# Kernel optimization log

Measured on AMD Instinct MI355X. Metric: run time of the kernel, lower is better.

Reference implementation:

```python
import jax, jax.numpy as jnp
import numpy as np

B, N, L, D = 1, 128, 256, 256   # batch, num_seqs, seq_len, msa_dim
P, H = 128, 8                   # pair_dim, num_heads
DH = D // H                     # head_dim


def setup_inputs() -> dict:
    key = jax.random.key(0)
    ks = jax.random.split(key, 7)
    msa = jax.random.normal(ks[0], (B, N, L, D), dtype=jnp.float32)
    pair = jax.random.normal(ks[1], (B, L, L, P), dtype=jnp.float32)
    mask = jax.random.randint(ks[2], (B, N, L), 0, 2) > 0  # bool key mask
    w_qkv = jax.random.normal(ks[3], (D, 3 * D), dtype=jnp.float32) * (D ** -0.5)
    w_pb = jax.random.normal(ks[4], (P, H), dtype=jnp.float32) * (P ** -0.5)
    b_pb = jnp.zeros((H,), dtype=jnp.float32)
    w_out = jax.random.normal(ks[5], (D, D), dtype=jnp.float32) * (D ** -0.5)
    b_out = jnp.zeros((D,), dtype=jnp.float32)
    return {"msa": msa, "pair": pair, "mask": mask, "w_qkv": w_qkv,
            "w_pb": w_pb, "b_pb": b_pb, "w_out": w_out, "b_out": b_out}


def reference(msa, pair, mask, w_qkv, w_pb, b_pb, w_out, b_out):
    b, n, l, d = msa.shape
    scaling = DH ** -0.5
    qkv = msa @ w_qkv                                   # [b,n,l,3d]
    qkv = qkv.reshape(b, n, l, 3, H, DH)
    q, k, v = qkv[..., 0, :, :], qkv[..., 1, :, :], qkv[..., 2, :, :]  # [b,n,l,h,dh]
    pair_bias = (pair @ w_pb + b_pb)                    # [b,l,l,h]
    pair_bias = jnp.transpose(pair_bias, (0, 3, 1, 2))  # [b,h,l,l]
    # scores: [b,n,h,l,l]
    dots = jnp.einsum('bnqhd,bnkhd->bnhqk', q, k) * scaling
    dots = dots + pair_bias[:, None]                    # broadcast over num_seqs
    dots = jnp.where(mask[:, :, None, None, :], dots, -jnp.inf)  # mask keys
    attn = jax.nn.softmax(dots, axis=-1)
    out = jnp.einsum('bnhqk,bnkhd->bnqhd', attn, v)     # [b,n,l,h,dh]
    out = out.reshape(b, n, l, d)
    return out @ w_out + b_out
```

## Files before the change

kernel.cpp:

```cpp
#include <hip/hip_runtime.h>
#include <hip/hip_bf16.h>

#define NN 128
#define LL 256
#define DD 256
#define PP 128
#define HH 8
#define DHH 32

typedef __bf16 bf16x8 __attribute__((ext_vector_type(8)));
typedef short s16x4 __attribute__((ext_vector_type(4)));
typedef float f32x4 __attribute__((ext_vector_type(4)));
typedef unsigned int u32x2 __attribute__((ext_vector_type(2)));

__device__ __forceinline__ void gload_lds16(const void* g, void* l) {
  __builtin_amdgcn_global_load_lds(
      (const __attribute__((address_space(1))) void*)g,
      (__attribute__((address_space(3))) void*)l, 16, 0, 0);
}

__global__ __launch_bounds__(256) void cvt_bf16(
    const float* __restrict__ src, __hip_bfloat16* __restrict__ dst, int n) {
  for (int i = (blockIdx.x * 256 + threadIdx.x) * 4; i < n; i += gridDim.x * 1024) {
    float4 v = *(const float4*)(src + i);
    ushort4 o;
    o.x = __bfloat16_as_ushort(__float2bfloat16(v.x));
    o.y = __bfloat16_as_ushort(__float2bfloat16(v.y));
    o.z = __bfloat16_as_ushort(__float2bfloat16(v.z));
    o.w = __bfloat16_as_ushort(__float2bfloat16(v.w));
    *(ushort4*)(dst + i) = o;
  }
}

__global__ __launch_bounds__(256) void transpose_cvt(
    const float* __restrict__ src, __hip_bfloat16* __restrict__ dst,
    int K, int N) {
  __shared__ float t[32][33];
  int n0 = blockIdx.x * 32, k0 = blockIdx.y * 32;
  int tx = threadIdx.x & 31, ty = threadIdx.x >> 5;
  for (int i = 0; i < 4; ++i) {
    int ky = ty + i * 8;
    t[ky][tx] = src[(size_t)(k0 + ky) * N + n0 + tx];
  }
  __syncthreads();
  for (int i = 0; i < 4; ++i) {
    int ny = ty + i * 8;
    dst[(size_t)(n0 + ny) * K + k0 + tx] = __float2bfloat16(t[tx][ny]);
  }
}

#define MODE_I32 0
#define MODE_I8 1
#define MODE_BF16 2
#define MODE_F32 3

__global__ __launch_bounds__(256) void mask_expand(
    const unsigned char* __restrict__ mraw, float* __restrict__ mout) {
  __shared__ int s_or1, s_or2, s_or3, s_max, s_mode;
  int tid = threadIdx.x;
  if (tid == 0) { s_or1 = 0; s_or2 = 0; s_or3 = 0; s_max = 0; }
  __syncthreads();
  int or1 = 0, or2 = 0, or3 = 0, mx = 0;
  for (int j = tid; j < 4096; j += 256) {
    int b = mraw[j];
    mx = mx > b ? mx : b;
    int r = j & 3;
    if (r == 1) or1 |= b;
    else if (r == 2) or2 |= b;
    else if (r == 3) or3 |= b;
  }
  atomicOr(&s_or1, or1); atomicOr(&s_or2, or2); atomicOr(&s_or3, or3);
  atomicMax(&s_max, mx);
  __syncthreads();
  if (tid == 0) {
    int mode;
    if (s_max <= 1) mode = ((s_or1 | s_or2 | s_or3) == 0) ? MODE_I32 : MODE_I8;
    else            mode = (s_or1 != 0) ? MODE_BF16 : MODE_F32;
    s_mode = mode;
  }
  __syncthreads();
  int mode = s_mode;
  int i0 = blockIdx.x * 1024;
  for (int i = i0 + tid; i < i0 + 1024; i += 256) {
    int v;
    if (mode == MODE_I32)       v = ((const int*)mraw)[i] != 0;
    else if (mode == MODE_I8)   v = mraw[i] != 0;
    else if (mode == MODE_BF16) v = ((const unsigned short*)mraw)[i] != 0;
    else                        v = ((const unsigned int*)mraw)[i] != 0;
    mout[i] = v ? 1.f : 0.f;
  }
}

#define GEMM_MAINLOOP(Aptr, Btptr)                                            \
  __shared__ __align__(16) __hip_bfloat16 Asm[128 * 32];                      \
  __shared__ __align__(16) __hip_bfloat16 Bsm[128 * 32];                      \
  int tid = threadIdx.x;                                                      \
  int lane = tid & 63;                                                        \
  int wv = tid >> 6;                                                          \
  int wm = (wv >> 1) * 64, wn = (wv & 1) * 64;                                \
  int lr = lane & 15, quad = lane >> 4;                                       \
  int bm = blockIdx.x, bn = blockIdx.y;                                       \
  f32x4 acc[4][4];                                                            \
  for (int i = 0; i < 4; ++i)                                                 \
    for (int j = 0; j < 4; ++j) acc[i][j] = (f32x4){0.f, 0.f, 0.f, 0.f};      \
  for (int ks = 0; ks < 8; ++ks) {                                            \
    int k0 = ks * 32;                                                         \
    if (ks) __syncthreads();                                                  \
    for (int i = 0; i < 2; ++i) {                                             \
      int c = tid + i * 256;                                                  \
      int row = c >> 2, cc = c & 3;                                           \
      int ldsbase = (wv * 64 + i * 256) * 8;      \
      gload_lds16(Aptr + ((size_t)(bm * 128 + row)) * 256 + k0 + cc * 8,      \
                  Asm + ldsbase);                                             \
      gload_lds16(Btptr + ((size_t)(bn * 128 + row)) * 256 + k0 + cc * 8,     \
                  Bsm + ldsbase);                                             \
    }                                                                         \
    __syncthreads();                                                          \
    bf16x8 af[4], bfr[4];                                                     \
    for (int mi = 0; mi < 4; ++mi)                                            \
      af[mi] = *(const bf16x8*)&Asm[(wm + mi * 16 + lr) * 32 + quad * 8];     \
    for (int ni = 0; ni < 4; ++ni)                                            \
      bfr[ni] = *(const bf16x8*)&Bsm[(wn + ni * 16 + lr) * 32 + quad * 8];    \
    for (int mi = 0; mi < 4; ++mi)                                            \
      for (int ni = 0; ni < 4; ++ni)                                          \
        acc[mi][ni] = __builtin_amdgcn_mfma_f32_16x16x32_bf16(                \
            af[mi], bfr[ni], acc[mi][ni], 0, 0, 0);                           \
  }

__global__ __launch_bounds__(256) void qkv_gemm_mfma(
    const __hip_bfloat16* __restrict__ A,
    const __hip_bfloat16* __restrict__ Bt,
    __hip_bfloat16* __restrict__ qb,
    __hip_bfloat16* __restrict__ kb,
    __hip_bfloat16* __restrict__ vb) {
  GEMM_MAINLOOP(A, Bt)
  for (int mi = 0; mi < 4; ++mi) {
    for (int ni = 0; ni < 4; ++ni) {
      int gcol = bn * 128 + wn + ni * 16 + lr;
      int t = gcol >> 8, rem = gcol & 255;
      int h = rem >> 5, dh = rem & 31;
      for (int r = 0; r < 4; ++r) {
        int grow = bm * 128 + wm + mi * 16 + quad * 4 + r;
        int n = grow >> 8, l = grow & 255;
        __hip_bfloat16 val = __float2bfloat16(acc[mi][ni][r]);
        if (t == 0)
          qb[(size_t)(((n * HH + h) * LL + l)) * DHH + dh] = val;
        else if (t == 1)
          kb[(size_t)(((n * HH + h) * LL + l)) * DHH + dh] = val;
        else
          vb[(size_t)(((n * HH + h) * DHH + dh)) * LL + l] = val;
      }
    }
  }
}

__global__ __launch_bounds__(256) void out_gemm_mfma(
    const __hip_bfloat16* __restrict__ A,
    const __hip_bfloat16* __restrict__ Bt,
    const float* __restrict__ bout,
    float* __restrict__ C) {
  GEMM_MAINLOOP(A, Bt)
  for (int mi = 0; mi < 4; ++mi) {
    for (int ni = 0; ni < 4; ++ni) {
      int gcol = bn * 128 + wn + ni * 16 + lr;
      float bo = bout[gcol];
      for (int r = 0; r < 4; ++r) {
        int grow = bm * 128 + wm + mi * 16 + quad * 4 + r;
        C[(size_t)grow * 256 + gcol] = acc[mi][ni][r] + bo;
      }
    }
  }
}

__global__ __launch_bounds__(256) void pair_bias_kernel(
    const float* __restrict__ pair,
    const float* __restrict__ w_pb,
    const float* __restrict__ b_pb,
    __hip_bfloat16* __restrict__ expb) {
  __shared__ float wp[128][9];
  __shared__ float rows[32][129];
  int tid = threadIdx.x;
  for (int i = 0; i < 4; ++i) {
    int e = tid + i * 256;
    wp[e >> 3][e & 7] = w_pb[e];
  }
  int row0 = blockIdx.x * 32;
  const float* src = pair + (size_t)row0 * PP;
  for (int i = 0; i < 16; ++i) {
    int e = tid + i * 256;
    int r = e >> 7, c = e & 127;
    rows[r][c] = src[r * 128 + c];
  }
  __syncthreads();
  int h = tid >> 5, rl = tid & 31;
  float acc = b_pb[h] - 12.0f;
  for (int p = 0; p < 128; ++p)
    acc += rows[rl][p] * wp[p][h];
  int row = row0 + rl;
  int i = row >> 8, j = row & 255;
  expb[((size_t)(h * LL + i)) * LL + j] = __float2bfloat16(__expf(acc));
}

__global__ __launch_bounds__(256, 2) void attn_mfma(
    const __hip_bfloat16* __restrict__ qb,
    const __hip_bfloat16* __restrict__ kb,
    const __hip_bfloat16* __restrict__ vbt,
    const __hip_bfloat16* __restrict__ expb,
    const float* __restrict__ maskf,
    __hip_bfloat16* __restrict__ ao) {
  int bx = blockIdx.x;
  int h = bx >> 7, n = bx & 127;
  int nh = n * HH + h;
  int tid = threadIdx.x, lane = tid & 63, wv = tid >> 6;
  int lr = lane & 15, quad = lane >> 4;
  int wm = wv * 64;
  size_t base = (size_t)nh * (LL * DHH);

  const __hip_bfloat16* qp = qb + base;
  const __hip_bfloat16* kp = kb + base;
  const __hip_bfloat16* vp = vbt + base;
  const __hip_bfloat16* ep = expb + (size_t)h * LL * LL;
  const float* mrow = maskf + n * LL;

  const float cs = 0.17677669529663687f * 1.4426950408889634f;

  bf16x8 aq[4];
#pragma unroll
  for (int mi = 0; mi < 4; ++mi)
    aq[mi] = *(const bf16x8*)(qp + (size_t)(wm + mi * 16 + lr) * DHH + quad * 8);

  bf16x8 bkA[4], bkB[4];
  s16x4 avA[4][2], avB[4][2];
  f32x4 mwA[4], mwB[4];
  uint2 ebE[4], ebO[4];

#define LOADKT(S, KT)                                                          \
  {                                                                            \
    const int j0_ = (KT) * 64;                                                 \
    _Pragma("unroll") for (int nj = 0; nj < 4; ++nj)                           \
        bk##S[nj] =                                                            \
        *(const bf16x8*)(kp + (size_t)(j0_ + nj * 16 + lr) * DHH + quad * 8);  \
    _Pragma("unroll") for (int nj = 0; nj < 4; ++nj) {                         \
      av##S[nj][0] = *(const s16x4*)(vp + (size_t)lr * LL +                    \
                                     j0_ + nj * 16 + quad * 4);                \
      av##S[nj][1] = *(const s16x4*)(vp + (size_t)(16 + lr) * LL +             \
                                     j0_ + nj * 16 + quad * 4);                \
    }                                                                          \
    _Pragma("unroll") for (int nj = 0; nj < 4; ++nj)                           \
        mw##S[nj] = *(const f32x4*)(mrow + j0_ + nj * 16 + quad * 4);          \
  }

#define LOADEB(S, KT, MI)                                                      \
  {                                                                            \
    const __hip_bfloat16* er_ =                                                \
        ep + (size_t)(wm + (MI) * 16 + lr) * LL + (KT) * 64;                   \
    _Pragma("unroll") for (int nj = 0; nj < 4; ++nj)                           \
        eb##S[nj] = *(const uint2*)(er_ + nj * 16 + quad * 4);                 \
  }

#define MI_PHASE(KT, MI, C, EC, EN, NKT, NMI, DOPF)                            \
  {                                                                            \
    if (DOPF) LOADEB(EN, NKT, NMI);                                            \
    f32x4 s_[4];                                                               \
    _Pragma("unroll") for (int nj = 0; nj < 4; ++nj)                           \
        s_[nj] = __builtin_amdgcn_mfma_f32_16x16x32_bf16(                      \
            bk##C[nj], aq[MI], (f32x4){0.f, 0.f, 0.f, 0.f}, 0, 0, 0);          \
    _Pragma("unroll") for (int nj = 0; nj < 4; ++nj) {                         \
      uint2 e_ = eb##EC[nj];                                                   \
      f32x4 m4_ = mw##C[nj];                                                   \
      float em0_ = __uint_as_float(e_.x << 16) * m4_[0];                       \
      float em1_ = __uint_as_float(e_.x & 0xffff0000u) * m4_[1];               \
      float em2_ = __uint_as_float(e_.y << 16) * m4_[2];                       \
      float em3_ = __uint_as_float(e_.y & 0xffff0000u) * m4_[3];               \
      float p0_ = exp2f(s_[nj][0] * cs) * em0_;                                \
      float p1_ = exp2f(s_[nj][1] * cs) * em1_;                                \
      float p2_ = exp2f(s_[nj][2] * cs) * em2_;                                \
      float p3_ = exp2f(s_[nj][3] * cs) * em3_;                                \
      lsum[MI] += (p0_ + p1_) + (p2_ + p3_);                                   \
      unsigned lo_ =                                                           \
          ((unsigned)__bfloat16_as_ushort(__float2bfloat16(p1_)) << 16) |      \
          (unsigned)__bfloat16_as_ushort(__float2bfloat16(p0_));               \
      unsigned hi_ =                                                           \
          ((unsigned)__bfloat16_as_ushort(__float2bfloat16(p3_)) << 16) |      \
          (unsigned)__bfloat16_as_ushort(__float2bfloat16(p2_));               \
      u32x2 pu_ = {lo_, hi_};                                                  \
      s16x4 pb_ = __builtin_bit_cast(s16x4, pu_);                              \
      o_acc[MI][0] = __builtin_amdgcn_mfma_f32_16x16x16bf16_1k(                \
          av##C[nj][0], pb_, o_acc[MI][0], 0, 0, 0);                           \
      o_acc[MI][1] = __builtin_amdgcn_mfma_f32_16x16x16bf16_1k(                \
          av##C[nj][1], pb_, o_acc[MI][1], 0, 0, 0);                           \
    }                                                                          \
  }

#define KT_PHASE(KT, C, N, LAST)                                               \
  {                                                                            \
    if (!(LAST)) LOADKT(N, (KT) + 1);                                          \
    MI_PHASE(KT, 0, C, E, O, KT, 1, 1)                                         \
    MI_PHASE(KT, 1, C, O, E, KT, 2, 1)                                         \
    MI_PHASE(KT, 2, C, E, O, KT, 3, 1)                                         \
    MI_PHASE(KT, 3, C, O, E, (KT) + 1 > 3 ? 0 : (KT) + 1, 0, !(LAST))          \
  }

  float lsum[4] = {0.f, 0.f, 0.f, 0.f};
  f32x4 o_acc[4][2];
#pragma unroll
  for (int mi = 0; mi < 4; ++mi)
#pragma unroll
    for (int no = 0; no < 2; ++no) o_acc[mi][no] = (f32x4){0.f, 0.f, 0.f, 0.f};

  LOADKT(A, 0)
  LOADEB(E, 0, 0)

  KT_PHASE(0, A, B, 0)
  KT_PHASE(1, B, A, 0)
  KT_PHASE(2, A, B, 0)
  KT_PHASE(3, B, A, 1)

#undef LOADKT
#undef LOADEB
#undef MI_PHASE
#undef KT_PHASE

#pragma unroll
  for (int mi = 0; mi < 4; ++mi) {
    float ls = lsum[mi];
    ls += __shfl_xor(ls, 16);
    ls += __shfl_xor(ls, 32);
    float inv = (ls > 0.f) ? 1.f / ls : 0.f;
    int q = wm + mi * 16 + lr;
#pragma unroll
    for (int no = 0; no < 2; ++no) {
      f32x4 o = o_acc[mi][no];
      ushort4 w;
      w.x = __bfloat16_as_ushort(__float2bfloat16(o[0] * inv));
      w.y = __bfloat16_as_ushort(__float2bfloat16(o[1] * inv));
      w.z = __bfloat16_as_ushort(__float2bfloat16(o[2] * inv));
      w.w = __bfloat16_as_ushort(__float2bfloat16(o[3] * inv));
      *(ushort4*)(ao + (size_t)n * (LL * DD) + (size_t)q * DD +
                  h * DHH + no * 16 + quad * 4) = w;
    }
  }
}

extern "C" void kernel_launch(void* const* d_in, const int* in_sizes, int n_in,
                              void* d_out, int out_size, void* d_ws, size_t ws_size,
                              hipStream_t stream) {
  const float* msa   = (const float*)d_in[0];
  const float* pair  = (const float*)d_in[1];
  const unsigned char* mask = (const unsigned char*)d_in[2];
  const float* w_qkv = (const float*)d_in[3];
  const float* w_pb  = (const float*)d_in[4];
  const float* b_pb  = (const float*)d_in[5];
  const float* w_out = (const float*)d_in[6];
  const float* b_out = (const float*)d_in[7];
  float* out = (float*)d_out;

  char* ws = (char*)d_ws;
  __hip_bfloat16* qb      = (__hip_bfloat16*)(ws);
  __hip_bfloat16* kb      = (__hip_bfloat16*)(ws + 16777216);
  __hip_bfloat16* vb      = (__hip_bfloat16*)(ws + 33554432);
  __hip_bfloat16* msa_c   = (__hip_bfloat16*)(ws + 50331648);
  __hip_bfloat16* ao      = (__hip_bfloat16*)(ws + 50331648);
  __hip_bfloat16* expb    = (__hip_bfloat16*)(ws + 67108864);
  __hip_bfloat16* wqkv_t  = (__hip_bfloat16*)(ws + 71303168);
  __hip_bfloat16* wout_t  = (__hip_bfloat16*)(ws + 71696384);
  float*          msk     = (float*)(ws + 71827456);

  mask_expand<<<32, 256, 0, stream>>>(mask, msk);
  cvt_bf16<<<1024, 256, 0, stream>>>(msa, msa_c, NN * LL * DD);
  transpose_cvt<<<dim3(24, 8), 256, 0, stream>>>(w_qkv, wqkv_t, 256, 768);
  transpose_cvt<<<dim3(8, 8), 256, 0, stream>>>(w_out, wout_t, 256, 256);

  qkv_gemm_mfma<<<dim3(256, 6), 256, 0, stream>>>(msa_c, wqkv_t, qb, kb, vb);
  pair_bias_kernel<<<2048, 256, 0, stream>>>(pair, w_pb, b_pb, expb);
  attn_mfma<<<1024, 256, 0, stream>>>(qb, kb, vb, expb, msk, ao);
  out_gemm_mfma<<<dim3(256, 2), 256, 0, stream>>>(ao, wout_t, b_out, out);
}
```

Before: 252.9 us.

## Permute key index layout so attention loads use 16-byte vector reads

```diff
diff --git a/kernel.cpp b/kernel.cpp
--- a/kernel.cpp
+++ b/kernel.cpp
@@ -10,8 +10,13 @@
 
 typedef __bf16 bf16x8 __attribute__((ext_vector_type(8)));
 typedef short s16x4 __attribute__((ext_vector_type(4)));
+typedef short s16x8 __attribute__((ext_vector_type(8)));
 typedef float f32x4 __attribute__((ext_vector_type(4)));
 typedef unsigned int u32x2 __attribute__((ext_vector_type(2)));
+
+__device__ __forceinline__ int permk(int k) {
+  return (k & 0xC3) | ((k & 0x30) >> 2) | ((k & 0x0C) << 2);
+}
 
 __device__ __forceinline__ void gload_lds16(const void* g, void* l) {
   __builtin_amdgcn_global_load_lds(
@@ -87,7 +92,7 @@
     else if (mode == MODE_I8)   v = mraw[i] != 0;
     else if (mode == MODE_BF16) v = ((const unsigned short*)mraw)[i] != 0;
     else                        v = ((const unsigned int*)mraw)[i] != 0;
-    mout[i] = v ? 1.f : 0.f;
+    mout[(i & ~255) | permk(i & 255)] = v ? 1.f : 0.f;
   }
 }
 
@@ -148,7 +153,7 @@
         else if (t == 1)
           kb[(size_t)(((n * HH + h) * LL + l)) * DHH + dh] = val;
         else
-          vb[(size_t)(((n * HH + h) * DHH + dh)) * LL + l] = val;
+          vb[(size_t)(((n * HH + h) * DHH + dh)) * LL + permk(l)] = val;
       }
     }
   }
@@ -198,7 +203,7 @@
     acc += rows[rl][p] * wp[p][h];
   int row = row0 + rl;
   int i = row >> 8, j = row & 255;
-  expb[((size_t)(h * LL + i)) * LL + j] = __float2bfloat16(__expf(acc));
+  expb[((size_t)(h * LL + i)) * LL + permk(j)] = __float2bfloat16(__expf(acc));
 }
 
 __global__ __launch_bounds__(256, 2) void attn_mfma(
@@ -230,9 +235,10 @@
     aq[mi] = *(const bf16x8*)(qp + (size_t)(wm + mi * 16 + lr) * DHH + quad * 8);
 
   bf16x8 bkA[4], bkB[4];
-  s16x4 avA[4][2], avB[4][2];
-  f32x4 mwA[4], mwB[4];
-  uint2 ebE[4], ebO[4];
+  s16x8 avA0a, avA0b, avA1a, avA1b;
+  s16x8 avB0a, avB0b, avB1a, avB1b;
+  uint4 e0a, e0b, e1a, e1b, e2a, e2b, e3a, e3b;
+  f32x4 mw0, mw1, mw2, mw3;
 
 #define LOADKT(S, KT)                                                          \
   {                                                                            \
@@ -240,65 +246,81 @@
     _Pragma("unroll") for (int nj = 0; nj < 4; ++nj)                           \
         bk##S[nj] =                                                            \
         *(const bf16x8*)(kp + (size_t)(j0_ + nj * 16 + lr) * DHH + quad * 8);  \
-    _Pragma("unroll") for (int nj = 0; nj < 4; ++nj) {                         \
-      av##S[nj][0] = *(const s16x4*)(vp + (size_t)lr * LL +                    \
-                                     j0_ + nj * 16 + quad * 4);                \
-      av##S[nj][1] = *(const s16x4*)(vp + (size_t)(16 + lr) * LL +             \
-                                     j0_ + nj * 16 + quad * 4);                \
-    }                                                                          \
-    _Pragma("unroll") for (int nj = 0; nj < 4; ++nj)                           \
-        mw##S[nj] = *(const f32x4*)(mrow + j0_ + nj * 16 + quad * 4);          \
-  }
-
-#define LOADEB(S, KT, MI)                                                      \
-  {                                                                            \
-    const __hip_bfloat16* er_ =                                                \
-        ep + (size_t)(wm + (MI) * 16 + lr) * LL + (KT) * 64;                   \
-    _Pragma("unroll") for (int nj = 0; nj < 4; ++nj)                           \
-        eb##S[nj] = *(const uint2*)(er_ + nj * 16 + quad * 4);                 \
-  }
-
-#define MI_PHASE(KT, MI, C, EC, EN, NKT, NMI, DOPF)                            \
-  {                                                                            \
-    if (DOPF) LOADEB(EN, NKT, NMI);                                            \
-    f32x4 s_[4];                                                               \
-    _Pragma("unroll") for (int nj = 0; nj < 4; ++nj)                           \
-        s_[nj] = __builtin_amdgcn_mfma_f32_16x16x32_bf16(                      \
-            bk##C[nj], aq[MI], (f32x4){0.f, 0.f, 0.f, 0.f}, 0, 0, 0);          \
-    _Pragma("unroll") for (int nj = 0; nj < 4; ++nj) {                         \
-      uint2 e_ = eb##EC[nj];                                                   \
-      f32x4 m4_ = mw##C[nj];                                                   \
-      float em0_ = __uint_as_float(e_.x << 16) * m4_[0];                       \
-      float em1_ = __uint_as_float(e_.x & 0xffff0000u) * m4_[1];               \
-      float em2_ = __uint_as_float(e_.y << 16) * m4_[2];                       \
-      float em3_ = __uint_as_float(e_.y & 0xffff0000u) * m4_[3];               \
-      float p0_ = exp2f(s_[nj][0] * cs) * em0_;                                \
-      float p1_ = exp2f(s_[nj][1] * cs) * em1_;                                \
-      float p2_ = exp2f(s_[nj][2] * cs) * em2_;                                \
-      float p3_ = exp2f(s_[nj][3] * cs) * em3_;                                \
-      lsum[MI] += (p0_ + p1_) + (p2_ + p3_);                                   \
-      unsigned lo_ =                                                           \
-          ((unsigned)__bfloat16_as_ushort(__float2bfloat16(p1_)) << 16) |      \
-          (unsigned)__bfloat16_as_ushort(__float2bfloat16(p0_));               \
-      unsigned hi_ =                                                           \
-          ((unsigned)__bfloat16_as_ushort(__float2bfloat16(p3_)) << 16) |      \
-          (unsigned)__bfloat16_as_ushort(__float2bfloat16(p2_));               \
-      u32x2 pu_ = {lo_, hi_};                                                  \
-      s16x4 pb_ = __builtin_bit_cast(s16x4, pu_);                              \
-      o_acc[MI][0] = __builtin_amdgcn_mfma_f32_16x16x16bf16_1k(                \
-          av##C[nj][0], pb_, o_acc[MI][0], 0, 0, 0);                           \
-      o_acc[MI][1] = __builtin_amdgcn_mfma_f32_16x16x16bf16_1k(                \
-          av##C[nj][1], pb_, o_acc[MI][1], 0, 0, 0);                           \
-    }                                                                          \
+    av##S##0a = *(const s16x8*)(vp + (size_t)lr * LL + j0_ + quad * 16);       \
+    av##S##0b = *(const s16x8*)(vp + (size_t)lr * LL + j0_ + quad * 16 + 8);   \
+    av##S##1a = *(const s16x8*)(vp + (size_t)(16 + lr) * LL + j0_ + quad * 16);\
+    av##S##1b =                                                                \
+        *(const s16x8*)(vp + (size_t)(16 + lr) * LL + j0_ + quad * 16 + 8);    \
+  }
+
+#define LOADEB_ALL(KT)                                                         \
+  {                                                                            \
+    const int j0_ = (KT) * 64;                                                 \
+    e0a = *(const uint4*)(ep + (size_t)(wm + 0 + lr) * LL + j0_ + quad * 16);  \
+    e0b = *(const uint4*)(ep + (size_t)(wm + 0 + lr) * LL + j0_ + quad * 16 + 8);\
+    e1a = *(const uint4*)(ep + (size_t)(wm + 16 + lr) * LL + j0_ + quad * 16); \
+    e1b = *(const uint4*)(ep + (size_t)(wm + 16 + lr) * LL + j0_ + quad * 16 + 8);\
+    e2a = *(const uint4*)(ep + (size_t)(wm + 32 + lr) * LL + j0_ + quad * 16); \
+    e2b = *(const uint4*)(ep + (size_t)(wm + 32 + lr) * LL + j0_ + quad * 16 + 8);\
+    e3a = *(const uint4*)(ep + (size_t)(wm + 48 + lr) * LL + j0_ + quad * 16); \
+    e3b = *(const uint4*)(ep + (size_t)(wm + 48 + lr) * LL + j0_ + quad * 16 + 8);\
+  }
+
+#define LOADMW(KT)                                                             \
+  {                                                                            \
+    const int j0_ = (KT) * 64;                                                 \
+    mw0 = *(const f32x4*)(mrow + j0_ + quad * 16 + 0);                         \
+    mw1 = *(const f32x4*)(mrow + j0_ + quad * 16 + 4);                         \
+    mw2 = *(const f32x4*)(mrow + j0_ + quad * 16 + 8);                         \
+    mw3 = *(const f32x4*)(mrow + j0_ + quad * 16 + 12);                        \
+  }
+
+#define NJ_STEP(C, MI, NJ, EX, EY, AV0, AV1, LO)                               \
+  {                                                                            \
+    f32x4 s_ = __builtin_amdgcn_mfma_f32_16x16x32_bf16(                        \
+        bk##C[NJ], aq[MI], (f32x4){0.f, 0.f, 0.f, 0.f}, 0, 0, 0);              \
+    float em0_ = __uint_as_float((EX) << 16) * mw##NJ[0];                      \
+    float em1_ = __uint_as_float((EX) & 0xffff0000u) * mw##NJ[1];              \
+    float em2_ = __uint_as_float((EY) << 16) * mw##NJ[2];                      \
+    float em3_ = __uint_as_float((EY) & 0xffff0000u) * mw##NJ[3];              \
+    float p0_ = exp2f(s_[0] * cs) * em0_;                                      \
+    float p1_ = exp2f(s_[1] * cs) * em1_;                                      \
+    float p2_ = exp2f(s_[2] * cs) * em2_;                                      \
+    float p3_ = exp2f(s_[3] * cs) * em3_;                                      \
+    lsum[MI] += (p0_ + p1_) + (p2_ + p3_);                                     \
+    unsigned lo_ =                                                             \
+        ((unsigned)__bfloat16_as_ushort(__float2bfloat16(p1_)) << 16) |        \
+        (unsigned)__bfloat16_as_ushort(__float2bfloat16(p0_));                 \
+    unsigned hi_ =                                                             \
+        ((unsigned)__bfloat16_as_ushort(__float2bfloat16(p3_)) << 16) |        \
+        (unsigned)__bfloat16_as_ushort(__float2bfloat16(p2_));                 \
+    u32x2 pu_ = {lo_, hi_};                                                    \
+    s16x4 pb_ = __builtin_bit_cast(s16x4, pu_);                                \
+    s16x4 a0_ = __builtin_shufflevector(AV0, AV0, LO, LO + 1, LO + 2, LO + 3); \
+    s16x4 a1_ = __builtin_shufflevector(AV1, AV1, LO, LO + 1, LO + 2, LO + 3); \
+    o_acc[MI][0] = __builtin_amdgcn_mfma_f32_16x16x16bf16_1k(                  \
+        a0_, pb_, o_acc[MI][0], 0, 0, 0);                                      \
+    o_acc[MI][1] = __builtin_amdgcn_mfma_f32_16x16x16bf16_1k(                  \
+        a1_, pb_, o_acc[MI][1], 0, 0, 0);                                      \
+  }
+
+#define MI_PHASE(MI, C, EA, EB_)                                               \
+  {                                                                            \
+    NJ_STEP(C, MI, 0, EA.x, EA.y, av##C##0a, av##C##1a, 0)                     \
+    NJ_STEP(C, MI, 1, EA.z, EA.w, av##C##0a, av##C##1a, 4)                     \
+    NJ_STEP(C, MI, 2, EB_.x, EB_.y, av##C##0b, av##C##1b, 0)                   \
+    NJ_STEP(C, MI, 3, EB_.z, EB_.w, av##C##0b, av##C##1b, 4)                   \
   }
 
 #define KT_PHASE(KT, C, N, LAST)                                               \
   {                                                                            \
-    if (!(LAST)) LOADKT(N, (KT) + 1);                                          \
-    MI_PHASE(KT, 0, C, E, O, KT, 1, 1)                                         \
-    MI_PHASE(KT, 1, C, O, E, KT, 2, 1)                                         \
-    MI_PHASE(KT, 2, C, E, O, KT, 3, 1)                                         \
-    MI_PHASE(KT, 3, C, O, E, (KT) + 1 > 3 ? 0 : (KT) + 1, 0, !(LAST))          \
+    LOADEB_ALL(KT)                                                             \
+    LOADMW(KT)                                                                 \
+    if (!(LAST)) LOADKT(N, (KT) + 1)                                           \
+    MI_PHASE(0, C, e0a, e0b)                                                   \
+    MI_PHASE(1, C, e1a, e1b)                                                   \
+    MI_PHASE(2, C, e2a, e2b)                                                   \
+    MI_PHASE(3, C, e3a, e3b)                                                   \
   }
 
   float lsum[4] = {0.f, 0.f, 0.f, 0.f};
@@ -309,7 +331,6 @@
     for (int no = 0; no < 2; ++no) o_acc[mi][no] = (f32x4){0.f, 0.f, 0.f, 0.f};
 
   LOADKT(A, 0)
-  LOADEB(E, 0, 0)
 
   KT_PHASE(0, A, B, 0)
   KT_PHASE(1, B, A, 0)
@@ -317,7 +338,9 @@
   KT_PHASE(3, B, A, 1)
 
 #undef LOADKT
-#undef LOADEB
+#undef LOADEB_ALL
+#undef LOADMW
+#undef NJ_STEP
 #undef MI_PHASE
 #undef KT_PHASE
 
```

Measured after the change: 241.7 us. -4.5%, faster.
